# Performance work log

Measured on AMD Instinct MI355X. Metric: run time of the kernel, lower is better.

Reference implementation:

```python
import jax, jax.numpy as jnp
import numpy as np

N_NODES = 8192
N_EDGES = 524288
D_IN = 256
D_OUT = 256


def setup_inputs() -> dict:
    key = jax.random.key(0)
    ks = jax.random.split(key, 8)
    h = jax.random.normal(ks[0], (N_NODES, D_IN), dtype=jnp.float32)
    # Xavier-uniform-like scale for weights
    s = (6.0 / (D_IN + D_OUT)) ** 0.5
    W = jax.random.uniform(ks[1], (D_IN, D_OUT), jnp.float32, -s, s)
    Wq = jax.random.uniform(ks[2], (D_IN, D_OUT), jnp.float32, -s, s)
    bq = jnp.zeros((D_OUT,), jnp.float32)
    Wk = jax.random.uniform(ks[3], (D_IN, D_OUT), jnp.float32, -s, s)
    bk = jnp.zeros((D_OUT,), jnp.float32)
    senders = jax.random.randint(ks[4], (N_EDGES,), 0, N_NODES, dtype=jnp.int64 if jax.config.jax_enable_x64 else jnp.int32)
    receivers = jax.random.randint(ks[5], (N_EDGES,), 0, N_NODES, dtype=jnp.int64 if jax.config.jax_enable_x64 else jnp.int32)
    return {"h": h, "W": W, "Wq": Wq, "bq": bq, "Wk": Wk, "bk": bk,
            "senders": senders, "receivers": receivers}


def reference(h, W, Wq, bq, Wk, bk, senders, receivers):
    # Projected node features: (N, D_OUT)
    h_proj = jnp.dot(h, W)
    # Dense attention logits a = q @ k^T: (N, N), as in the original module
    q = jnp.dot(h, Wq) + bq
    k = jnp.dot(h, Wk) + bk
    a = jnp.dot(q, k.T)
    # Gather per-edge messages and attention weights, weight, scatter-add
    messages = h_proj[senders] * a[senders, receivers][:, None]  # (E, D_OUT)
    aggregated = jax.ops.segment_sum(messages, receivers, num_segments=h.shape[0])
    return jax.nn.relu(aggregated)
```

## Files before the change

kernel.cpp:

```cpp
#include <hip/hip_runtime.h>
#include <stdint.h>

typedef unsigned short u16;
typedef unsigned int u32;
typedef short v8s __attribute__((ext_vector_type(8)));
typedef float v4f __attribute__((ext_vector_type(4)));

#define N_NODES 8192
#define N_EDGES 524288
#define DFEAT 256
#define PAD 160

typedef __attribute__((address_space(3))) void lds_t;
typedef const __attribute__((address_space(1))) void gbl_t;

static __device__ __forceinline__ float bflo(u32 u) { return __uint_as_float(u << 16); }
static __device__ __forceinline__ float bfhi(u32 u) { return __uint_as_float(u & 0xffff0000u); }
static __device__ __forceinline__ u16 f2bf(float f) {
    u32 u = __float_as_uint(f);
    u32 r = (u + 0x7fffu + ((u >> 16) & 1u)) >> 16;
    return (u16)r;
}

__global__ void prep(const float* __restrict__ h,
                     const float* __restrict__ w0, const float* __restrict__ w1,
                     const float* __restrict__ w2,
                     const int* __restrict__ recv, const int* __restrict__ send,
                     u16* __restrict__ hb, u16* __restrict__ wt,
                     int* __restrict__ cnt, int* __restrict__ es_pad) {
    __shared__ u16 t[64][65];
    int b = blockIdx.x;
    if (b < 2048) {
        int i = (b * 256 + threadIdx.x) * 4;
        float4 v = *(const float4*)(h + i);
        uint2 p;
        p.x = (u32)f2bf(v.x) | ((u32)f2bf(v.y) << 16);
        p.y = (u32)f2bf(v.z) | ((u32)f2bf(v.w) << 16);
        *(uint2*)(hb + i) = p;
    } else if (b < 2096) {
        int bb = b - 2048;
        int region = bb >> 4;
        int tile = bb & 15;
        int k0 = (tile >> 2) * 64, n0 = (tile & 3) * 64;
        const float* w = (region == 0) ? w0 : ((region == 1) ? w1 : w2);
        int tx = threadIdx.x & 63, ty = threadIdx.x >> 6;
#pragma unroll
        for (int it = 0; it < 16; it++) {
            int row = it * 4 + ty;
            t[row][tx] = f2bf(w[(k0 + row) * 256 + n0 + tx]);
        }
        __syncthreads();
        u16* o = wt + region * 65536;
#pragma unroll
        for (int it = 0; it < 16; it++) {
            int row = it * 4 + ty;
            o[(n0 + row) * 256 + k0 + tx] = t[tx][row];
        }
    } else {
        int e = (b - 2096) * 256 + threadIdx.x;
        int r = recv[e];
        int pos = atomicAdd(&cnt[r], 1);
        if (pos < PAD) es_pad[r * PAD + pos] = send[e];
    }
}

__global__ __launch_bounds__(256) void gemm_proj(
    const u16* __restrict__ h, const u16* __restrict__ wt,
    const float* __restrict__ bq, const float* __restrict__ bk,
    u16* __restrict__ hproj, u16* __restrict__ qb, u16* __restrict__ kb) {
    int wave = threadIdx.x >> 6;
    int lane = threadIdx.x & 63;
    int lm = lane & 15;
    int lq = lane >> 4;
    int m0 = blockIdx.x * 64 + wave * 16;
    int region = blockIdx.y >> 2;
    int n0b = (blockIdx.y & 3) * 64;
    const u16* wtr = wt + region * 65536;

    v4f acc[4];
#pragma unroll
    for (int nt = 0; nt < 4; nt++) acc[nt] = (v4f){0.f, 0.f, 0.f, 0.f};

    const u16* arow = h + (m0 + lm) * 256 + lq * 8;
#pragma unroll
    for (int k0 = 0; k0 < 256; k0 += 32) {
        v8s a = *(const v8s*)(arow + k0);
#pragma unroll
        for (int nt = 0; nt < 4; nt++) {
            v8s b = *(const v8s*)(wtr + (n0b + nt * 16 + lm) * 256 + k0 + lq * 8);
            acc[nt] = __builtin_amdgcn_mfma_f32_16x16x32_bf16(a, b, acc[nt], 0, 0, 0);
        }
    }

    u16* outp = (region == 0) ? hproj : ((region == 1) ? qb : kb);
    const float* bias = (region == 1) ? bq : ((region == 2) ? bk : nullptr);
#pragma unroll
    for (int nt = 0; nt < 4; nt++) {
        int n = n0b + nt * 16 + lm;
        float bv = bias ? bias[n] : 0.f;
#pragma unroll
        for (int i = 0; i < 4; i++) {
            int m = m0 + lq * 4 + i;
            outp[m * 256 + n] = f2bf(acc[nt][i] + bv);
        }
    }
}

__global__ __launch_bounds__(256) void edge_fused(
    const u16* __restrict__ qb, const u16* __restrict__ kb, const u16* __restrict__ hpb,
    const int* __restrict__ cnt, const int* __restrict__ es_pad,
    float* __restrict__ out) {
    __shared__ char lds[65536];
    __shared__ float sc[4][16];
    int wave = threadIdx.x >> 6;
    int lane = threadIdx.x & 63;
    int r = blockIdx.x * 4 + wave;
    int lm = lane & 15, lq = lane >> 4;
    int lh = lane & 31, half = lane >> 5;
    int n = min(cnt[r], PAD);
    int base = r * PAD;
    char* qtile = lds + wave * 16384;
    char* htile = qtile + 8192;
    const char* qg = (const char*)qb;
    const char* hg = (const char*)hpb;

    v8s kf[8];
    const u16* krow = kb + r * 256 + lq * 8;
#pragma unroll
    for (int t = 0; t < 8; t++) kf[t] = *(const v8s*)(krow + t * 32);

    float a[8];
#pragma unroll
    for (int i = 0; i < 8; i++) a[i] = 0.f;

    for (int c0 = 0; c0 < n; c0 += 16) {
        int jq = c0 + lm;
        if (jq >= n) jq = n - 1;
        int sq = es_pad[base + jq];

        long qoff = (long)sq * 512 + lq * 16;
#pragma unroll
        for (int t = 0; t < 8; t++)
            __builtin_amdgcn_global_load_lds((gbl_t*)(qg + qoff + t * 64),
                                             (lds_t*)(qtile + t * 1024), 16, 0, 0);
#pragma unroll
        for (int u = 0; u < 8; u++) {
            int sh = __shfl(sq, 2 * u + half, 64);
            __builtin_amdgcn_global_load_lds((gbl_t*)(hg + (long)sh * 512 + lh * 16),
                                             (lds_t*)(htile + u * 1024), 16, 0, 0);
        }
        __asm volatile("s_waitcnt vmcnt(0)" ::: "memory");

        v4f acc = (v4f){0.f, 0.f, 0.f, 0.f};
#pragma unroll
        for (int t = 0; t < 8; t++) {
            v8s av = *(const v8s*)(qtile + t * 1024 + lane * 16);
            acc = __builtin_amdgcn_mfma_f32_16x16x32_bf16(av, kf[t], acc, 0, 0, 0);
        }
        if (lm == 0) {
#pragma unroll
            for (int i = 0; i < 4; i++) sc[wave][lq * 4 + i] = acc[i];
        }
        __threadfence_block();

        int m = n - c0;
        if (m >= 16) {
#pragma unroll
            for (int t0 = 0; t0 < 8; t0++) {
                float p = sc[wave][2 * t0 + half];
                uint4 hv = *(const uint4*)(htile + t0 * 1024 + half * 512 + lh * 16);
                a[0] += p * bflo(hv.x); a[1] += p * bfhi(hv.x);
                a[2] += p * bflo(hv.y); a[3] += p * bfhi(hv.y);
                a[4] += p * bflo(hv.z); a[5] += p * bfhi(hv.z);
                a[6] += p * bflo(hv.w); a[7] += p * bfhi(hv.w);
            }
        } else {
            for (int t = half; t < m; t += 2) {
                float p = sc[wave][t];
                uint4 hv = *(const uint4*)(htile + (t >> 1) * 1024 + (t & 1) * 512 + lh * 16);
                a[0] += p * bflo(hv.x); a[1] += p * bfhi(hv.x);
                a[2] += p * bflo(hv.y); a[3] += p * bfhi(hv.y);
                a[4] += p * bflo(hv.z); a[5] += p * bfhi(hv.z);
                a[6] += p * bflo(hv.w); a[7] += p * bfhi(hv.w);
            }
        }
    }

#pragma unroll
    for (int i = 0; i < 8; i++) a[i] += __shfl_xor(a[i], 32, 64);

    if (half == 0) {
        float4 o0, o1;
        o0.x = fmaxf(a[0], 0.f); o0.y = fmaxf(a[1], 0.f);
        o0.z = fmaxf(a[2], 0.f); o0.w = fmaxf(a[3], 0.f);
        o1.x = fmaxf(a[4], 0.f); o1.y = fmaxf(a[5], 0.f);
        o1.z = fmaxf(a[6], 0.f); o1.w = fmaxf(a[7], 0.f);
        float* op = out + r * 256 + lh * 8;
        *(float4*)op = o0;
        *(float4*)(op + 4) = o1;
    }
}

extern "C" void kernel_launch(void* const* d_in, const int* in_sizes, int n_in,
                              void* d_out, int out_size, void* d_ws, size_t ws_size,
                              hipStream_t stream) {
    const float* h  = (const float*)d_in[0];
    const float* W  = (const float*)d_in[1];
    const float* Wq = (const float*)d_in[2];
    const float* bq = (const float*)d_in[3];
    const float* Wk = (const float*)d_in[4];
    const float* bk = (const float*)d_in[5];
    const int* senders   = (const int*)d_in[6];
    const int* receivers = (const int*)d_in[7];
    float* out = (float*)d_out;

    char* ws = (char*)d_ws;
    u16* wt     = (u16*)ws;
    u16* hb     = (u16*)(ws + 393216);
    u16* hproj  = hb + N_NODES * DFEAT;
    u16* qb     = hproj + N_NODES * DFEAT;
    u16* kb     = qb + N_NODES * DFEAT;
    int* cnt    = (int*)(kb + N_NODES * DFEAT);
    int* es_pad = cnt + N_NODES;

    hipMemsetAsync(cnt, 0, N_NODES * sizeof(int), stream);
    prep<<<4144, 256, 0, stream>>>(h, W, Wq, Wk, receivers, senders, hb, wt, cnt, es_pad);
    gemm_proj<<<dim3(128, 12), 256, 0, stream>>>(hb, wt, bq, bk, hproj, qb, kb);
    edge_fused<<<N_NODES / 4, 256, 0, stream>>>(qb, kb, hproj, cnt, es_pad, out);
}
```

Baseline: 190.2 us.

## Fuse h bf16 conversion into GEMM, split edge rows across two waves

Drops the separate fp32-to-bf16 pass over h. The projection GEMM now loads fp32 h and converts it in registers, and the prep kernel only handles edge bucketing and weight transposes. The edge kernel replaces the LDS staging through global_load_lds with direct register loads of q and h_proj rows. It also splits each receiver's edge chunks across two waves, whose partial sums are combined through shared memory and a block barrier. The aim is less memory traffic and more parallelism per receiver, at the cost of more register pressure, a __syncthreads, and the GEMM reading h in fp32 twelve times (once per column-tile block).

```diff
diff --git a/kernel.cpp b/kernel.cpp
--- a/kernel.cpp
+++ b/kernel.cpp
@@ -10,9 +10,6 @@
 #define N_EDGES 524288
 #define DFEAT 256
 #define PAD 160
-
-typedef __attribute__((address_space(3))) void lds_t;
-typedef const __attribute__((address_space(1))) void gbl_t;
 
 static __device__ __forceinline__ float bflo(u32 u) { return __uint_as_float(u << 16); }
 static __device__ __forceinline__ float bfhi(u32 u) { return __uint_as_float(u & 0xffff0000u); }
@@ -22,22 +19,19 @@
     return (u16)r;
 }
 
-__global__ void prep(const float* __restrict__ h,
-                     const float* __restrict__ w0, const float* __restrict__ w1,
+__global__ void prep(const float* __restrict__ w0, const float* __restrict__ w1,
                      const float* __restrict__ w2,
                      const int* __restrict__ recv, const int* __restrict__ send,
-                     u16* __restrict__ hb, u16* __restrict__ wt,
+                     u16* __restrict__ wt,
                      int* __restrict__ cnt, int* __restrict__ es_pad) {
     __shared__ u16 t[64][65];
     int b = blockIdx.x;
     if (b < 2048) {
-        int i = (b * 256 + threadIdx.x) * 4;
-        float4 v = *(const float4*)(h + i);
-        uint2 p;
-        p.x = (u32)f2bf(v.x) | ((u32)f2bf(v.y) << 16);
-        p.y = (u32)f2bf(v.z) | ((u32)f2bf(v.w) << 16);
-        *(uint2*)(hb + i) = p;
-    } else if (b < 2096) {
+        int e = b * 256 + threadIdx.x;
+        int r = recv[e];
+        int pos = atomicAdd(&cnt[r], 1);
+        if (pos < PAD) es_pad[r * PAD + pos] = send[e];
+    } else {
         int bb = b - 2048;
         int region = bb >> 4;
         int tile = bb & 15;
@@ -56,16 +50,11 @@
             int row = it * 4 + ty;
             o[(n0 + row) * 256 + k0 + tx] = t[tx][row];
         }
-    } else {
-        int e = (b - 2096) * 256 + threadIdx.x;
-        int r = recv[e];
-        int pos = atomicAdd(&cnt[r], 1);
-        if (pos < PAD) es_pad[r * PAD + pos] = send[e];
     }
 }
 
 __global__ __launch_bounds__(256) void gemm_proj(
-    const u16* __restrict__ h, const u16* __restrict__ wt,
+    const float* __restrict__ h, const u16* __restrict__ wt,
     const float* __restrict__ bq, const float* __restrict__ bk,
     u16* __restrict__ hproj, u16* __restrict__ qb, u16* __restrict__ kb) {
     int wave = threadIdx.x >> 6;
@@ -81,10 +70,16 @@
 #pragma unroll
     for (int nt = 0; nt < 4; nt++) acc[nt] = (v4f){0.f, 0.f, 0.f, 0.f};
 
-    const u16* arow = h + (m0 + lm) * 256 + lq * 8;
+    const float* arow = h + (m0 + lm) * 256 + lq * 8;
 #pragma unroll
     for (int k0 = 0; k0 < 256; k0 += 32) {
-        v8s a = *(const v8s*)(arow + k0);
+        float4 u0 = *(const float4*)(arow + k0);
+        float4 u1 = *(const float4*)(arow + k0 + 4);
+        v8s a;
+        a[0] = (short)f2bf(u0.x); a[1] = (short)f2bf(u0.y);
+        a[2] = (short)f2bf(u0.z); a[3] = (short)f2bf(u0.w);
+        a[4] = (short)f2bf(u1.x); a[5] = (short)f2bf(u1.y);
+        a[6] = (short)f2bf(u1.z); a[7] = (short)f2bf(u1.w);
 #pragma unroll
         for (int nt = 0; nt < 4; nt++) {
             v8s b = *(const v8s*)(wtr + (n0b + nt * 16 + lm) * 256 + k0 + lq * 8);
@@ -110,19 +105,16 @@
     const u16* __restrict__ qb, const u16* __restrict__ kb, const u16* __restrict__ hpb,
     const int* __restrict__ cnt, const int* __restrict__ es_pad,
     float* __restrict__ out) {
-    __shared__ char lds[65536];
     __shared__ float sc[4][16];
+    __shared__ float comb[2][64][8];
     int wave = threadIdx.x >> 6;
     int lane = threadIdx.x & 63;
-    int r = blockIdx.x * 4 + wave;
+    int rl = wave >> 1, part = wave & 1;
+    int r = blockIdx.x * 2 + rl;
     int lm = lane & 15, lq = lane >> 4;
     int lh = lane & 31, half = lane >> 5;
     int n = min(cnt[r], PAD);
     int base = r * PAD;
-    char* qtile = lds + wave * 16384;
-    char* htile = qtile + 8192;
-    const char* qg = (const char*)qb;
-    const char* hg = (const char*)hpb;
 
     v8s kf[8];
     const u16* krow = kb + r * 256 + lq * 8;
@@ -133,71 +125,75 @@
 #pragma unroll
     for (int i = 0; i < 8; i++) a[i] = 0.f;
 
-    for (int c0 = 0; c0 < n; c0 += 16) {
+    for (int c0 = part * 16; c0 < n; c0 += 32) {
         int jq = c0 + lm;
         if (jq >= n) jq = n - 1;
         int sq = es_pad[base + jq];
 
-        long qoff = (long)sq * 512 + lq * 16;
-#pragma unroll
-        for (int t = 0; t < 8; t++)
-            __builtin_amdgcn_global_load_lds((gbl_t*)(qg + qoff + t * 64),
-                                             (lds_t*)(qtile + t * 1024), 16, 0, 0);
+        const u16* qrow = qb + (long)sq * 256 + lq * 8;
+        v8s qf[8];
+#pragma unroll
+        for (int t = 0; t < 8; t++) qf[t] = *(const v8s*)(qrow + t * 32);
+        uint4 hv[8];
 #pragma unroll
         for (int u = 0; u < 8; u++) {
             int sh = __shfl(sq, 2 * u + half, 64);
-            __builtin_amdgcn_global_load_lds((gbl_t*)(hg + (long)sh * 512 + lh * 16),
-                                             (lds_t*)(htile + u * 1024), 16, 0, 0);
-        }
-        __asm volatile("s_waitcnt vmcnt(0)" ::: "memory");
+            hv[u] = *(const uint4*)(hpb + (long)sh * 256 + lh * 8);
+        }
 
         v4f acc = (v4f){0.f, 0.f, 0.f, 0.f};
 #pragma unroll
-        for (int t = 0; t < 8; t++) {
-            v8s av = *(const v8s*)(qtile + t * 1024 + lane * 16);
-            acc = __builtin_amdgcn_mfma_f32_16x16x32_bf16(av, kf[t], acc, 0, 0, 0);
-        }
+        for (int t = 0; t < 8; t++)
+            acc = __builtin_amdgcn_mfma_f32_16x16x32_bf16(qf[t], kf[t], acc, 0, 0, 0);
         if (lm == 0) {
 #pragma unroll
             for (int i = 0; i < 4; i++) sc[wave][lq * 4 + i] = acc[i];
         }
         __threadfence_block();
 
-        int m = n - c0;
+        int m = n - c0; if (m > 16) m = 16;
         if (m >= 16) {
 #pragma unroll
-            for (int t0 = 0; t0 < 8; t0++) {
-                float p = sc[wave][2 * t0 + half];
-                uint4 hv = *(const uint4*)(htile + t0 * 1024 + half * 512 + lh * 16);
-                a[0] += p * bflo(hv.x); a[1] += p * bfhi(hv.x);
-                a[2] += p * bflo(hv.y); a[3] += p * bfhi(hv.y);
-                a[4] += p * bflo(hv.z); a[5] += p * bfhi(hv.z);
-                a[6] += p * bflo(hv.w); a[7] += p * bfhi(hv.w);
+            for (int u = 0; u < 8; u++) {
+                float p = sc[wave][2 * u + half];
+                uint4 hu = hv[u];
+                a[0] += p * bflo(hu.x); a[1] += p * bfhi(hu.x);
+                a[2] += p * bflo(hu.y); a[3] += p * bfhi(hu.y);
+                a[4] += p * bflo(hu.z); a[5] += p * bfhi(hu.z);
+                a[6] += p * bflo(hu.w); a[7] += p * bfhi(hu.w);
             }
         } else {
             for (int t = half; t < m; t += 2) {
                 float p = sc[wave][t];
-                uint4 hv = *(const uint4*)(htile + (t >> 1) * 1024 + (t & 1) * 512 + lh * 16);
-                a[0] += p * bflo(hv.x); a[1] += p * bfhi(hv.x);
-                a[2] += p * bflo(hv.y); a[3] += p * bfhi(hv.y);
-                a[4] += p * bflo(hv.z); a[5] += p * bfhi(hv.z);
-                a[6] += p * bflo(hv.w); a[7] += p * bfhi(hv.w);
+                uint4 hu = hv[t >> 1];
+                a[0] += p * bflo(hu.x); a[1] += p * bfhi(hu.x);
+                a[2] += p * bflo(hu.y); a[3] += p * bfhi(hu.y);
+                a[4] += p * bflo(hu.z); a[5] += p * bfhi(hu.z);
+                a[6] += p * bflo(hu.w); a[7] += p * bfhi(hu.w);
             }
         }
     }
 
-#pragma unroll
-    for (int i = 0; i < 8; i++) a[i] += __shfl_xor(a[i], 32, 64);
-
-    if (half == 0) {
-        float4 o0, o1;
-        o0.x = fmaxf(a[0], 0.f); o0.y = fmaxf(a[1], 0.f);
-        o0.z = fmaxf(a[2], 0.f); o0.w = fmaxf(a[3], 0.f);
-        o1.x = fmaxf(a[4], 0.f); o1.y = fmaxf(a[5], 0.f);
-        o1.z = fmaxf(a[6], 0.f); o1.w = fmaxf(a[7], 0.f);
-        float* op = out + r * 256 + lh * 8;
-        *(float4*)op = o0;
-        *(float4*)(op + 4) = o1;
+    if (part == 1) {
+#pragma unroll
+        for (int i = 0; i < 8; i++) comb[rl][lane][i] = a[i];
+    }
+    __syncthreads();
+    if (part == 0) {
+#pragma unroll
+        for (int i = 0; i < 8; i++) a[i] += comb[rl][lane][i];
+#pragma unroll
+        for (int i = 0; i < 8; i++) a[i] += __shfl_xor(a[i], 32, 64);
+        if (half == 0) {
+            float4 o0, o1;
+            o0.x = fmaxf(a[0], 0.f); o0.y = fmaxf(a[1], 0.f);
+            o0.z = fmaxf(a[2], 0.f); o0.w = fmaxf(a[3], 0.f);
+            o1.x = fmaxf(a[4], 0.f); o1.y = fmaxf(a[5], 0.f);
+            o1.z = fmaxf(a[6], 0.f); o1.w = fmaxf(a[7], 0.f);
+            float* op = out + r * 256 + lh * 8;
+            *(float4*)op = o0;
+            *(float4*)(op + 4) = o1;
+        }
     }
 }
 
@@ -216,15 +212,14 @@
 
     char* ws = (char*)d_ws;
     u16* wt     = (u16*)ws;
-    u16* hb     = (u16*)(ws + 393216);
-    u16* hproj  = hb + N_NODES * DFEAT;
+    u16* hproj  = (u16*)(ws + 393216);
     u16* qb     = hproj + N_NODES * DFEAT;
     u16* kb     = qb + N_NODES * DFEAT;
     int* cnt    = (int*)(kb + N_NODES * DFEAT);
     int* es_pad = cnt + N_NODES;
 
     hipMemsetAsync(cnt, 0, N_NODES * sizeof(int), stream);
-    prep<<<4144, 256, 0, stream>>>(h, W, Wq, Wk, receivers, senders, hb, wt, cnt, es_pad);
-    gemm_proj<<<dim3(128, 12), 256, 0, stream>>>(hb, wt, bq, bk, hproj, qb, kb);
-    edge_fused<<<N_NODES / 4, 256, 0, stream>>>(qb, kb, hproj, cnt, es_pad, out);
-}
+    prep<<<2096, 256, 0, stream>>>(W, Wq, Wk, receivers, senders, wt, cnt, es_pad);
+    gemm_proj<<<dim3(128, 12), 256, 0, stream>>>(h, wt, bq, bk, hproj, qb, kb);
+    edge_fused<<<N_NODES / 2, 256, 0, stream>>>(qb, kb, hproj, cnt, es_pad, out);
+}
```

After: 255.4 us. 1.34x slower.
